# Kernel optimization log

Measured on AMD Instinct MI355X. Metric: run time of the kernel, lower is better.

Reference implementation:

```python
import jax, jax.numpy as jnp
import numpy as np

N = 100000
IN_DIM, H1, H2, OUT_DIM = 128, 128, 16, 10
DROP_P = 0.5


def setup_inputs() -> dict:
    key = jax.random.key(0)
    ks = jax.random.split(key, 9)
    x = jax.random.normal(ks[0], (N, IN_DIM), dtype=jnp.float32)
    edge_index = jax.random.randint(ks[1], (2, 1600000), 0, N, dtype=jnp.int64)
    s = lambda k, sh, fan: jax.random.normal(k, sh, jnp.float32) * (1.0 / np.sqrt(fan))
    return {
        "x": x,
        "edge_index": edge_index,
        "W1": s(ks[2], (IN_DIM, H1), IN_DIM),
        "b1": jnp.zeros((H1,), jnp.float32),
        "W2": s(ks[3], (H1, H2), H1),
        "b2": jnp.zeros((H2,), jnp.float32),
        "prelu_a": jnp.array(0.25, jnp.float32),  # nn.PReLU(): single shared parameter
        "Wfc": s(ks[4], (H2, OUT_DIM), H2),
        "bfc": jnp.zeros((OUT_DIM,), jnp.float32),
    }


def _prelu(x, a):
    return jnp.where(x >= 0, x, a * x)


def _dropout(x, key, p=DROP_P):
    keep = jax.random.bernoulli(key, 1.0 - p, x.shape)
    return jnp.where(keep, x / (1.0 - p), 0.0)


def _gcn_norm(edge_index, n):
    # PyG GCNConv default: add self-loops, symmetric deg^-1/2 normalization
    loop = jnp.arange(n, dtype=edge_index.dtype)
    src = jnp.concatenate([edge_index[0], loop])
    dst = jnp.concatenate([edge_index[1], loop])
    deg = jax.ops.segment_sum(jnp.ones_like(src, jnp.float32), dst, num_segments=n)
    dis = jnp.where(deg > 0, jax.lax.rsqrt(deg), 0.0)
    norm = dis[src] * dis[dst]  # [E + N]
    return src, dst, norm


def _gcn_conv(h, src, dst, norm, b, n):
    msg = h[src] * norm[:, None]          # gather + per-edge scale
    agg = jax.ops.segment_sum(msg, dst, num_segments=n)  # scatter-add
    return agg + b


def reference(x, edge_index, W1, b1, W2, b2, prelu_a, Wfc, bfc):
    n = x.shape[0]
    src, dst, norm = _gcn_norm(edge_index, n)
    dk1, dk2 = jax.random.split(jax.random.key(42))
    h = _gcn_conv(x @ W1, src, dst, norm, b1, n)
    h = _dropout(_prelu(h, prelu_a), dk1)
    h = _gcn_conv(h @ W2, src, dst, norm, b2, n)
    h = _dropout(_prelu(h, prelu_a), dk2)
    return h @ Wfc + bfc
```

## Files before the change

kernel.cpp:

```cpp
#include <hip/hip_runtime.h>
#include <stdint.h>

#define G1  128
#define BSH 9
#define BSZ 512

typedef __attribute__((ext_vector_type(8))) _Float16 f16x8;
typedef __attribute__((ext_vector_type(2))) _Float16 f16x2;
typedef __attribute__((ext_vector_type(2))) __fp16 fp16x2r;
typedef __attribute__((ext_vector_type(4))) float f32x4;

#define TF_ROUND(x0, x1, r)                                                    \
  {                                                                            \
    x0 += x1;                                                                  \
    x1 = (x1 << r) | (x1 >> (32 - r));                                         \
    x1 ^= x0;                                                                  \
  }

__host__ __device__ inline void threefry2x32(uint32_t k0, uint32_t k1,
                                             uint32_t x0, uint32_t x1,
                                             uint32_t* o0, uint32_t* o1) {
  uint32_t ks2 = k0 ^ k1 ^ 0x1BD11BDAu;
  x0 += k0; x1 += k1;
  TF_ROUND(x0, x1, 13) TF_ROUND(x0, x1, 15) TF_ROUND(x0, x1, 26) TF_ROUND(x0, x1, 6)
  x0 += k1; x1 += ks2 + 1u;
  TF_ROUND(x0, x1, 17) TF_ROUND(x0, x1, 29) TF_ROUND(x0, x1, 16) TF_ROUND(x0, x1, 24)
  x0 += ks2; x1 += k0 + 2u;
  TF_ROUND(x0, x1, 13) TF_ROUND(x0, x1, 15) TF_ROUND(x0, x1, 26) TF_ROUND(x0, x1, 6)
  x0 += k0; x1 += k1 + 3u;
  TF_ROUND(x0, x1, 17) TF_ROUND(x0, x1, 29) TF_ROUND(x0, x1, 16) TF_ROUND(x0, x1, 24)
  x0 += k1; x1 += ks2 + 4u;
  TF_ROUND(x0, x1, 13) TF_ROUND(x0, x1, 15) TF_ROUND(x0, x1, 26) TF_ROUND(x0, x1, 6)
  x0 += ks2; x1 += k0 + 5u;
  *o0 = x0; *o1 = x1;
}

__device__ inline uint32_t tf_bits32(uint32_t k0, uint32_t k1, uint32_t ctr) {
  uint32_t a, b;
  threefry2x32(k0, k1, 0u, ctr, &a, &b);
  return a ^ b;
}

__device__ inline f16x2 u2h(uint32_t u) {
  union { uint32_t u; f16x2 h; } c; c.u = u; return c.h;
}
__device__ inline uint32_t h2u(f16x2 h) {
  union { uint32_t u; f16x2 h; } c; c.h = h; return c.u;
}
__device__ inline uint32_t pk2h(float a, float b) {
  union { fp16x2r h; uint32_t u; } c;
  c.h = __builtin_amdgcn_cvt_pkrtz(a, b);
  return c.u;
}
__device__ inline uint16_t f2h(float a) {
  union { fp16x2r h; uint32_t u; } c;
  c.h = __builtin_amdgcn_cvt_pkrtz(a, 0.f);
  return (uint16_t)c.u;
}

__global__ __launch_bounds__(256) void k_hist(const int* __restrict__ dst,
                                              int* __restrict__ hist_t,
                                              int E, int NB, int chunk) {
  __shared__ int hist[256];
  const int tid = threadIdx.x;
  for (int b = tid; b < NB; b += 256) hist[b] = 0;
  __syncthreads();
  int e0 = blockIdx.x * chunk;
  int e1 = min(e0 + chunk, E);
  for (int e = e0 + tid; e < e1; e += 256)
    atomicAdd(&hist[dst[e] >> BSH], 1);
  __syncthreads();
  for (int b = tid; b < NB; b += 256)
    hist_t[b * G1 + blockIdx.x] = hist[b];
}

__global__ __launch_bounds__(256) void k_bsc_gemm1(
    const int* __restrict__ src, const int* __restrict__ dst,
    const int* __restrict__ hist_t, int* __restrict__ segs,
    uint32_t* __restrict__ ebuf, int E, int NB, int chunk,
    const float* __restrict__ x, const float* __restrict__ W,
    uint16_t* __restrict__ h, int n) {
  __shared__ char smem[(64 * 136 + 128 * 136) * 2];
  const int tid = threadIdx.x;
  if (blockIdx.x < G1) {
    int* rowsum = (int*)smem;
    int* cur = ((int*)smem) + 256;
    const int g = blockIdx.x;
    int rs = 0, ps = 0;
    if (tid < NB) {
      const int* row = hist_t + tid * G1;
      for (int i = 0; i < G1; ++i) {
        int v = row[i];
        rs += v;
        if (i < g) ps += v;
      }
    }
    rowsum[tid] = rs;
    __syncthreads();
    for (int off = 1; off < 256; off <<= 1) {
      int tmp = (tid >= off) ? rowsum[tid - off] : 0;
      __syncthreads();
      rowsum[tid] += tmp;
      __syncthreads();
    }
    int rb = rowsum[tid] - rs;
    if (tid < NB) cur[tid] = rb + ps;
    if (g == 0) {
      if (tid < NB) segs[tid] = rb;
      if (tid == 255) segs[NB] = rowsum[255];
    }
    __syncthreads();
    int e0 = g * chunk, e1 = min(e0 + chunk, E);
    for (int e = e0 + tid; e < e1; e += 256) {
      int d = dst[e];
      int slot = atomicAdd(&cur[d >> BSH], 1);
      ebuf[slot] = ((uint32_t)src[e] << BSH) | (uint32_t)(d & (BSZ - 1));
    }
    return;
  }
  uint16_t (*As)[136] = (uint16_t(*)[136])smem;
  uint16_t (*Bs)[136] = (uint16_t(*)[136])(smem + 64 * 136 * 2);
  const int rowBase = (blockIdx.x - G1) * 64;
  for (int i = tid; i < 64 * 32; i += 256) {
    int r = i >> 5, c4 = i & 31;
    float4 v = make_float4(0.f, 0.f, 0.f, 0.f);
    if (rowBase + r < n)
      v = ((const float4*)(x + (size_t)(rowBase + r) * 128))[c4];
    *(uint2*)&As[r][c4 * 4] = make_uint2(pk2h(v.x, v.y), pk2h(v.z, v.w));
  }
  {
    int k2 = tid >> 7;
    int c = tid & 127;
    for (int kk = 0; kk < 128; kk += 4) {
      int k = kk + k2 * 2;
      *(uint32_t*)&Bs[c][k] = pk2h(W[k * 128 + c], W[(k + 1) * 128 + c]);
    }
  }
  __syncthreads();
  const int wid = tid >> 6;
  const int lane = tid & 63;
  const int l15 = lane & 15;
  const int lhi = lane >> 4;
  f32x4 acc[8];
#pragma unroll
  for (int t = 0; t < 8; ++t) acc[t] = (f32x4){0.f, 0.f, 0.f, 0.f};
  const int arow = wid * 16 + l15;
#pragma unroll
  for (int ks = 0; ks < 4; ++ks) {
    f16x8 a = *(f16x8*)&As[arow][ks * 32 + lhi * 8];
#pragma unroll
    for (int ct = 0; ct < 8; ++ct) {
      f16x8 bfrag = *(f16x8*)&Bs[ct * 16 + l15][ks * 32 + lhi * 8];
      acc[ct] = __builtin_amdgcn_mfma_f32_16x16x32_f16(a, bfrag, acc[ct], 0, 0, 0);
    }
  }
#pragma unroll
  for (int j = 0; j < 4; ++j) {
    int row = rowBase + wid * 16 + lhi * 4 + j;
    if (row < n) {
#pragma unroll
      for (int ct = 0; ct < 8; ++ct)
        h[(size_t)row * 128 + ct * 16 + l15] = f2h(acc[ct][j]);
    }
  }
}

__global__ __launch_bounds__(256) void k_bfinal(const uint32_t* __restrict__ ebuf,
                                                const int* __restrict__ segs,
                                                int* __restrict__ rowptr,
                                                float* __restrict__ dis,
                                                int* __restrict__ csrc,
                                                int n, int NB, int E) {
  __shared__ int cnt[BSZ];
  __shared__ int sc[256];
  int b = blockIdx.x;
  int t = threadIdx.x;
  int seg0 = segs[b];
  int seg1 = segs[b + 1];
  for (int i = t; i < BSZ; i += 256) cnt[i] = 0;
  __syncthreads();
  for (int i = seg0 + t; i < seg1; i += 256)
    atomicAdd(&cnt[ebuf[i] & (BSZ - 1)], 1);
  __syncthreads();
  int a0 = cnt[2 * t], a1 = cnt[2 * t + 1];
  int s = a0 + a1;
  sc[t] = s;
  __syncthreads();
  for (int off = 1; off < 256; off <<= 1) {
    int tmp = (t >= off) ? sc[t - off] : 0;
    __syncthreads();
    sc[t] += tmp;
    __syncthreads();
  }
  int pre = sc[t] - s;
  int node0 = b * BSZ;
  int p0 = seg0 + pre;
  int p1 = p0 + a0;
  int nd0 = node0 + 2 * t, nd1 = nd0 + 1;
  if (nd0 <= n) rowptr[nd0] = p0;
  if (nd1 <= n) rowptr[nd1] = p1;
  if (nd0 < n) dis[nd0] = rsqrtf((float)(a0 + 1));
  if (nd1 < n) dis[nd1] = rsqrtf((float)(a1 + 1));
  cnt[2 * t] = p0;
  cnt[2 * t + 1] = p1;
  __syncthreads();
  for (int i = seg0 + t; i < seg1; i += 256) {
    uint32_t u = ebuf[i];
    int slot = atomicAdd(&cnt[u & (BSZ - 1)], 1);
    csrc[slot] = (int)(u >> BSH);
  }
  if (b == NB - 1 && t == 0) rowptr[n] = E;
}

__global__ __launch_bounds__(256) void k_gather12(
    const int* __restrict__ rowptr, const int* __restrict__ csrc,
    const float* __restrict__ dis, const uint16_t* __restrict__ h1,
    const float* __restrict__ bias, const float* __restrict__ pa,
    const float* __restrict__ W2, uint32_t* __restrict__ h2,
    int n, uint32_t k0, uint32_t k1) {
  __shared__ uint16_t hs[16][136];
  __shared__ uint16_t Bs[16][136];
  const int tid = threadIdx.x;
  {
    int c = tid & 15;
    int k8 = tid >> 4;
#pragma unroll
    for (int jj = 0; jj < 8; ++jj) {
      int k = k8 * 8 + jj;
      Bs[c][k] = f2h(W2[k * 16 + c]);
    }
  }
  const int wid = tid >> 6;
  const int lane = tid & 63;
  const int q = lane >> 4;
  const int sl = lane & 15;
  const int f0 = 8 * sl + 2 * q;
  const int base = blockIdx.x * 16;
  const uint4* rowbase = (const uint4*)h1;
  const float a = pa[0];
  const float bi0 = bias[f0];
  const float bi1 = bias[f0 + 1];
  for (int i = 0; i < 4; ++i) {
    const int nrow = wid * 4 + i;
    const int v = base + nrow;
    if (v < n) {
      uint32_t jj = (uint32_t)v * 128u + (uint32_t)f0;
      uint32_t bits0 = tf_bits32(k0, k1, jj);
      uint32_t bits1 = tf_bits32(k0, k1, jj + 1);
      float dv = dis[v];
      f16x2 acc0 = u2h(0u), acc1 = u2h(0u), acc2 = u2h(0u), acc3 = u2h(0u);
      if (q == 0) {
        uint4 r = rowbase[(size_t)v * 16 + sl];
        f16x2 w = u2h(pk2h(dv, dv));
        acc0 += u2h(r.x) * w; acc1 += u2h(r.y) * w;
        acc2 += u2h(r.z) * w; acc3 += u2h(r.w) * w;
      }
      int beg = rowptr[v];
      int deg = rowptr[v + 1] - beg;
      for (int bb = 0; bb < deg; bb += 64) {
        int cnt = min(64, deg - bb);
        int idx = bb + lane;
        int sv = v;
        uint32_t wpk = 0u;
        if (idx < deg) {
          sv = csrc[beg + idx];
          float wd = dis[sv];
          wpk = pk2h(wd, wd);
        }
        for (int j = 0; j < cnt; j += 16) {
          int s0 = __shfl(sv, j + q);
          int s1 = __shfl(sv, j + 4 + q);
          int s2 = __shfl(sv, j + 8 + q);
          int s3 = __shfl(sv, j + 12 + q);
          uint32_t w0 = (uint32_t)__shfl((int)wpk, j + q);
          uint32_t w1 = (uint32_t)__shfl((int)wpk, j + 4 + q);
          uint32_t w2 = (uint32_t)__shfl((int)wpk, j + 8 + q);
          uint32_t w3 = (uint32_t)__shfl((int)wpk, j + 12 + q);
          uint4 r0 = rowbase[(size_t)s0 * 16 + sl];
          uint4 r1 = rowbase[(size_t)s1 * 16 + sl];
          uint4 r2 = rowbase[(size_t)s2 * 16 + sl];
          uint4 r3 = rowbase[(size_t)s3 * 16 + sl];
          f16x2 hw0 = u2h(w0), hw1 = u2h(w1), hw2 = u2h(w2), hw3 = u2h(w3);
          acc0 += u2h(r0.x) * hw0; acc1 += u2h(r0.y) * hw0;
          acc2 += u2h(r0.z) * hw0; acc3 += u2h(r0.w) * hw0;
          acc0 += u2h(r1.x) * hw1; acc1 += u2h(r1.y) * hw1;
          acc2 += u2h(r1.z) * hw1; acc3 += u2h(r1.w) * hw1;
          acc0 += u2h(r2.x) * hw2; acc1 += u2h(r2.y) * hw2;
          acc2 += u2h(r2.z) * hw2; acc3 += u2h(r2.w) * hw2;
          acc0 += u2h(r3.x) * hw3; acc1 += u2h(r3.y) * hw3;
          acc2 += u2h(r3.z) * hw3; acc3 += u2h(r3.w) * hw3;
        }
      }
#define COMB(A)                                                                \
  {                                                                            \
    uint32_t u_ = h2u(A);                                                      \
    A = A + u2h((uint32_t)__shfl_xor((int)u_, 16));                            \
    u_ = h2u(A);                                                               \
    A = A + u2h((uint32_t)__shfl_xor((int)u_, 32));                            \
  }
      COMB(acc0) COMB(acc1) COMB(acc2) COMB(acc3)
#undef COMB
      f16x2 p = (q == 0) ? acc0 : (q == 1) ? acc1 : (q == 2) ? acc2 : acc3;
      float v0 = (float)p.x * dv + bi0;
      float v1 = (float)p.y * dv + bi1;
      v0 = v0 >= 0.f ? v0 : a * v0;
      v1 = v1 >= 0.f ? v1 : a * v1;
      float r0 = (bits0 & 0x80000000u) ? 0.f : 2.f * v0;
      float r1 = (bits1 & 0x80000000u) ? 0.f : 2.f * v1;
      *(uint32_t*)&hs[nrow][f0] = pk2h(r0, r1);
    } else {
      *(uint32_t*)&hs[nrow][f0] = 0u;
    }
  }
  __syncthreads();
  if (wid == 0) {
    const int l15 = lane & 15;
    const int lhi = lane >> 4;
    f32x4 acc = (f32x4){0.f, 0.f, 0.f, 0.f};
#pragma unroll
    for (int ks = 0; ks < 4; ++ks) {
      f16x8 af = *(f16x8*)&hs[l15][ks * 32 + lhi * 8];
      f16x8 bf = *(f16x8*)&Bs[l15][ks * 32 + lhi * 8];
      acc = __builtin_amdgcn_mfma_f32_16x16x32_f16(af, bf, acc, 0, 0, 0);
    }
#pragma unroll
    for (int j = 0; j < 4; ++j) {
      int gnode = base + lhi * 4 + j;
      float val = acc[j];
      float pv = __shfl_xor(val, 1);
      if (gnode < n && (l15 & 1) == 0)
        h2[(size_t)gnode * 8 + (l15 >> 1)] = pk2h(val, pv);
    }
  }
}

__global__ __launch_bounds__(256) void k_gather2(
    const int* __restrict__ rowptr, const int* __restrict__ csrc,
    const float* __restrict__ dis, const uint32_t* __restrict__ h2,
    const float* __restrict__ bias, const float* __restrict__ pa,
    const float* __restrict__ Wfc, const float* __restrict__ bfc,
    float* __restrict__ out, int n, uint32_t k0, uint32_t k1) {
  __shared__ float wfc[16][10];
  __shared__ float sbfc[10];
  __shared__ float sval[32][16];
  const int tid = threadIdx.x;
  if (tid < 160) ((float*)wfc)[tid] = Wfc[tid];
  if (tid < 10) sbfc[tid] = bfc[tid];
  __syncthreads();
  const int gnode = (blockIdx.x * 256 + tid) >> 3;
  const int grp = tid >> 3;
  const int sub = tid & 7;
  const int q = sub >> 1;
  const int sl = sub & 1;
  const int f0 = 8 * sl + 2 * q;
  const uint4* rowbase = (const uint4*)h2;
  if (gnode < n) {
    uint32_t c0 = (uint32_t)gnode * 16u + (uint32_t)f0;
    uint32_t bits0 = tf_bits32(k0, k1, c0);
    uint32_t bits1 = tf_bits32(k0, k1, c0 + 1);
    float dv = dis[gnode];
    f16x2 acc0 = u2h(0u), acc1 = u2h(0u), acc2 = u2h(0u), acc3 = u2h(0u);
    if (q == 0) {
      uint4 r = rowbase[(size_t)gnode * 2 + sl];
      f16x2 w = u2h(pk2h(dv, dv));
      acc0 += u2h(r.x) * w; acc1 += u2h(r.y) * w;
      acc2 += u2h(r.z) * w; acc3 += u2h(r.w) * w;
    }
    int beg = rowptr[gnode];
    int deg = rowptr[gnode + 1] - beg;
    for (int bb = 0; bb < deg; bb += 8) {
      int cnt = min(8, deg - bb);
      int idx = bb + sub;
      int sv = gnode;
      uint32_t wpk = 0u;
      if (idx < deg) {
        sv = csrc[beg + idx];
        float wd = dis[sv];
        wpk = pk2h(wd, wd);
      }
      for (int j = 0; j < cnt; j += 4) {
        int s0 = __shfl(sv, j + q, 8);
        uint32_t w0 = (uint32_t)__shfl((int)wpk, j + q, 8);
        uint4 r0 = rowbase[(size_t)s0 * 2 + sl];
        f16x2 hw0 = u2h(w0);
        acc0 += u2h(r0.x) * hw0; acc1 += u2h(r0.y) * hw0;
        acc2 += u2h(r0.z) * hw0; acc3 += u2h(r0.w) * hw0;
      }
    }
#define COMB2(A)                                                               \
  {                                                                            \
    uint32_t u_ = h2u(A);                                                      \
    A = A + u2h((uint32_t)__shfl_xor((int)u_, 2));                             \
    u_ = h2u(A);                                                               \
    A = A + u2h((uint32_t)__shfl_xor((int)u_, 4));                             \
  }
    COMB2(acc0) COMB2(acc1) COMB2(acc2) COMB2(acc3)
#undef COMB2
    f16x2 p = (q == 0) ? acc0 : (q == 1) ? acc1 : (q == 2) ? acc2 : acc3;
    float a = pa[0];
    float v0 = (float)p.x * dv + bias[f0];
    float v1 = (float)p.y * dv + bias[f0 + 1];
    v0 = v0 >= 0.f ? v0 : a * v0;
    v1 = v1 >= 0.f ? v1 : a * v1;
    sval[grp][f0]     = (bits0 & 0x80000000u) ? 0.f : 2.f * v0;
    sval[grp][f0 + 1] = (bits1 & 0x80000000u) ? 0.f : 2.f * v1;
  }
  __syncthreads();
  if (gnode < n && sub < 5) {
    int c = sub * 2;
    float o0 = sbfc[c], o1 = sbfc[c + 1];
#pragma unroll
    for (int k = 0; k < 16; ++k) {
      float hv = sval[grp][k];
      o0 += hv * wfc[k][c];
      o1 += hv * wfc[k][c + 1];
    }
    *(float2*)&out[(size_t)gnode * 10 + c] = make_float2(o0, o1);
  }
}

extern "C" void kernel_launch(void* const* d_in, const int* in_sizes, int n_in,
                              void* d_out, int out_size, void* d_ws, size_t ws_size,
                              hipStream_t stream) {
  const float* x   = (const float*)d_in[0];
  const int*   ei  = (const int*)d_in[1];
  const float* W1  = (const float*)d_in[2];
  const float* b1  = (const float*)d_in[3];
  const float* W2  = (const float*)d_in[4];
  const float* b2  = (const float*)d_in[5];
  const float* pa  = (const float*)d_in[6];
  const float* Wfc = (const float*)d_in[7];
  const float* bfc = (const float*)d_in[8];
  float* out = (float*)d_out;

  const int n = in_sizes[0] / 128;
  const int E = in_sizes[1] / 2;
  const int* src = ei;
  const int* dst = ei + E;

  const int NB = (n + BSZ - 1) / BSZ;
  const int T = NB * G1;
  const int chunk = (E + G1 - 1) / G1;

  char* w = (char*)d_ws;
  auto alloc = [&](size_t bytes) {
    char* p = w;
    w += (bytes + 255) & ~(size_t)255;
    return p;
  };
  float* dis      = (float*)alloc((size_t)n * 4);
  int* rowptr     = (int*)alloc((size_t)(n + 1) * 4);
  int* hist_t     = (int*)alloc((size_t)(T + 1) * 4);
  int* segs       = (int*)alloc((size_t)(NB + 1) * 4);
  uint32_t* ebuf  = (uint32_t*)alloc((size_t)E * 4);
  int* csrc       = (int*)alloc((size_t)E * 4);
  uint16_t* h1f   = (uint16_t*)alloc((size_t)n * 128 * 2);
  uint32_t* h2f   = (uint32_t*)alloc((size_t)n * 8 * 4);

  uint32_t dk1_0, dk1_1, dk2_0, dk2_1;
  threefry2x32(0u, 42u, 0u, 0u, &dk1_0, &dk1_1);
  threefry2x32(0u, 42u, 0u, 1u, &dk2_0, &dk2_1);

  k_hist<<<G1, 256, 0, stream>>>(dst, hist_t, E, NB, chunk);
  k_bsc_gemm1<<<G1 + (n + 63) / 64, 256, 0, stream>>>(
      src, dst, hist_t, segs, ebuf, E, NB, chunk, x, W1, h1f, n);
  k_bfinal<<<NB, 256, 0, stream>>>(ebuf, segs, rowptr, dis, csrc, n, NB, E);

  k_gather12<<<(n + 15) / 16, 256, 0, stream>>>(rowptr, csrc, dis, h1f,
                                                b1, pa, W2, h2f, n, dk1_0, dk1_1);

  k_gather2<<<(n * 8 + 255) / 256, 256, 0, stream>>>(rowptr, csrc, dis, h2f,
                                                     b2, pa, Wfc, bfc, out, n,
                                                     dk2_0, dk2_1);
}
```

Measured before the change: 169.6 us.

## Split layer-1 gather into feature-sliced kernel and separate MFMA GEMM2

Replaces the fused gather+GEMM2 kernel with two kernels. The first gathers neighbour rows in 8 feature slices of 16 features each, where 8-lane groups handle one node per slice, so each slice's working set of h1 is smaller and more likely to stay in cache. It applies bias, PReLU and dropout, then writes a full f16 hidden activation to a new global buffer. The second kernel loads 64-row tiles of that buffer and runs the 128x16 GEMM with MFMA on all four waves. This trades extra global traffic (an n x 128 f16 round trip) and an extra launch for better cache locality in the gather and no idle waves in the GEMM.

```diff
diff --git a/kernel.cpp b/kernel.cpp
--- a/kernel.cpp
+++ b/kernel.cpp
@@ -212,15 +212,92 @@
   if (b == NB - 1 && t == 0) rowptr[n] = E;
 }
 
-__global__ __launch_bounds__(256) void k_gather12(
+__global__ __launch_bounds__(256) void k_gslice(
     const int* __restrict__ rowptr, const int* __restrict__ csrc,
     const float* __restrict__ dis, const uint16_t* __restrict__ h1,
     const float* __restrict__ bias, const float* __restrict__ pa,
-    const float* __restrict__ W2, uint32_t* __restrict__ h2,
-    int n, uint32_t k0, uint32_t k1) {
-  __shared__ uint16_t hs[16][136];
+    uint32_t* __restrict__ hbf, int n, uint32_t k0, uint32_t k1) {
+  const int slice = blockIdx.x & 7;
+  const int nblk = blockIdx.x >> 3;
+  const int tid = threadIdx.x;
+  const int grp = tid >> 3;
+  const int sub = tid & 7;
+  const int q = sub >> 1;
+  const int sl = sub & 1;
+  const int fo = slice * 16 + sl * 8 + q * 2;
+  const float a = pa[0];
+  const float bi0 = bias[fo], bi1 = bias[fo + 1];
+  const uint4* rowbase = (const uint4*)h1;
+  const int roff = slice * 2 + sl;
+  for (int i = 0; i < 4; ++i) {
+    const int v = nblk * 128 + grp * 4 + i;
+    if (v >= n) break;
+    uint32_t cc = (uint32_t)v * 128u + (uint32_t)fo;
+    uint32_t bits0 = tf_bits32(k0, k1, cc);
+    uint32_t bits1 = tf_bits32(k0, k1, cc + 1);
+    float dv = dis[v];
+    f16x2 acc0 = u2h(0u), acc1 = u2h(0u), acc2 = u2h(0u), acc3 = u2h(0u);
+    if (q == 0) {
+      uint4 r = rowbase[(size_t)v * 16 + roff];
+      f16x2 w = u2h(pk2h(dv, dv));
+      acc0 += u2h(r.x) * w; acc1 += u2h(r.y) * w;
+      acc2 += u2h(r.z) * w; acc3 += u2h(r.w) * w;
+    }
+    int beg = rowptr[v];
+    int deg = rowptr[v + 1] - beg;
+    for (int bb = 0; bb < deg; bb += 8) {
+      int cnt = min(8, deg - bb);
+      int idx = bb + sub;
+      int sv = v;
+      uint32_t wpk = 0u;
+      if (idx < deg) {
+        sv = csrc[beg + idx];
+        float wd = dis[sv];
+        wpk = pk2h(wd, wd);
+      }
+      for (int j = 0; j < cnt; j += 4) {
+        int s0 = __shfl(sv, j + q, 8);
+        uint32_t w0 = (uint32_t)__shfl((int)wpk, j + q, 8);
+        uint4 r0 = rowbase[(size_t)s0 * 16 + roff];
+        f16x2 hw = u2h(w0);
+        acc0 += u2h(r0.x) * hw; acc1 += u2h(r0.y) * hw;
+        acc2 += u2h(r0.z) * hw; acc3 += u2h(r0.w) * hw;
+      }
+    }
+#define COMB2(A)                                                               \
+  {                                                                            \
+    uint32_t u_ = h2u(A);                                                      \
+    A = A + u2h((uint32_t)__shfl_xor((int)u_, 2));                             \
+    u_ = h2u(A);                                                               \
+    A = A + u2h((uint32_t)__shfl_xor((int)u_, 4));                             \
+  }
+    COMB2(acc0) COMB2(acc1) COMB2(acc2) COMB2(acc3)
+#undef COMB2
+    f16x2 p = (q == 0) ? acc0 : (q == 1) ? acc1 : (q == 2) ? acc2 : acc3;
+    float v0 = (float)p.x * dv + bi0;
+    float v1 = (float)p.y * dv + bi1;
+    v0 = v0 >= 0.f ? v0 : a * v0;
+    v1 = v1 >= 0.f ? v1 : a * v1;
+    float r0 = (bits0 & 0x80000000u) ? 0.f : 2.f * v0;
+    float r1 = (bits1 & 0x80000000u) ? 0.f : 2.f * v1;
+    hbf[(size_t)v * 64 + slice * 8 + sl * 4 + q] = pk2h(r0, r1);
+  }
+}
+
+__global__ __launch_bounds__(256) void k_gemm2(const uint32_t* __restrict__ hbf,
+                                               const float* __restrict__ W2,
+                                               uint32_t* __restrict__ h2, int n) {
+  __shared__ uint16_t As[64][136];
   __shared__ uint16_t Bs[16][136];
   const int tid = threadIdx.x;
+  const int rowBase = blockIdx.x * 64;
+  for (int i = tid; i < 64 * 32; i += 256) {
+    int r = i >> 5, c4 = i & 31;
+    uint2 v = make_uint2(0u, 0u);
+    if (rowBase + r < n)
+      v = ((const uint2*)(hbf + (size_t)(rowBase + r) * 64))[c4];
+    *(uint2*)&As[r][c4 * 4] = v;
+  }
   {
     int c = tid & 15;
     int k8 = tid >> 4;
@@ -230,107 +307,26 @@
       Bs[c][k] = f2h(W2[k * 16 + c]);
     }
   }
+  __syncthreads();
   const int wid = tid >> 6;
   const int lane = tid & 63;
-  const int q = lane >> 4;
-  const int sl = lane & 15;
-  const int f0 = 8 * sl + 2 * q;
-  const int base = blockIdx.x * 16;
-  const uint4* rowbase = (const uint4*)h1;
-  const float a = pa[0];
-  const float bi0 = bias[f0];
-  const float bi1 = bias[f0 + 1];
-  for (int i = 0; i < 4; ++i) {
-    const int nrow = wid * 4 + i;
-    const int v = base + nrow;
-    if (v < n) {
-      uint32_t jj = (uint32_t)v * 128u + (uint32_t)f0;
-      uint32_t bits0 = tf_bits32(k0, k1, jj);
-      uint32_t bits1 = tf_bits32(k0, k1, jj + 1);
-      float dv = dis[v];
-      f16x2 acc0 = u2h(0u), acc1 = u2h(0u), acc2 = u2h(0u), acc3 = u2h(0u);
-      if (q == 0) {
-        uint4 r = rowbase[(size_t)v * 16 + sl];
-        f16x2 w = u2h(pk2h(dv, dv));
-        acc0 += u2h(r.x) * w; acc1 += u2h(r.y) * w;
-        acc2 += u2h(r.z) * w; acc3 += u2h(r.w) * w;
-      }
-      int beg = rowptr[v];
-      int deg = rowptr[v + 1] - beg;
-      for (int bb = 0; bb < deg; bb += 64) {
-        int cnt = min(64, deg - bb);
-        int idx = bb + lane;
-        int sv = v;
-        uint32_t wpk = 0u;
-        if (idx < deg) {
-          sv = csrc[beg + idx];
-          float wd = dis[sv];
-          wpk = pk2h(wd, wd);
-        }
-        for (int j = 0; j < cnt; j += 16) {
-          int s0 = __shfl(sv, j + q);
-          int s1 = __shfl(sv, j + 4 + q);
-          int s2 = __shfl(sv, j + 8 + q);
-          int s3 = __shfl(sv, j + 12 + q);
-          uint32_t w0 = (uint32_t)__shfl((int)wpk, j + q);
-          uint32_t w1 = (uint32_t)__shfl((int)wpk, j + 4 + q);
-          uint32_t w2 = (uint32_t)__shfl((int)wpk, j + 8 + q);
-          uint32_t w3 = (uint32_t)__shfl((int)wpk, j + 12 + q);
-          uint4 r0 = rowbase[(size_t)s0 * 16 + sl];
-          uint4 r1 = rowbase[(size_t)s1 * 16 + sl];
-          uint4 r2 = rowbase[(size_t)s2 * 16 + sl];
-          uint4 r3 = rowbase[(size_t)s3 * 16 + sl];
-          f16x2 hw0 = u2h(w0), hw1 = u2h(w1), hw2 = u2h(w2), hw3 = u2h(w3);
-          acc0 += u2h(r0.x) * hw0; acc1 += u2h(r0.y) * hw0;
-          acc2 += u2h(r0.z) * hw0; acc3 += u2h(r0.w) * hw0;
-          acc0 += u2h(r1.x) * hw1; acc1 += u2h(r1.y) * hw1;
-          acc2 += u2h(r1.z) * hw1; acc3 += u2h(r1.w) * hw1;
-          acc0 += u2h(r2.x) * hw2; acc1 += u2h(r2.y) * hw2;
-          acc2 += u2h(r2.z) * hw2; acc3 += u2h(r2.w) * hw2;
-          acc0 += u2h(r3.x) * hw3; acc1 += u2h(r3.y) * hw3;
-          acc2 += u2h(r3.z) * hw3; acc3 += u2h(r3.w) * hw3;
-        }
-      }
-#define COMB(A)                                                                \
-  {                                                                            \
-    uint32_t u_ = h2u(A);                                                      \
-    A = A + u2h((uint32_t)__shfl_xor((int)u_, 16));                            \
-    u_ = h2u(A);                                                               \
-    A = A + u2h((uint32_t)__shfl_xor((int)u_, 32));                            \
-  }
-      COMB(acc0) COMB(acc1) COMB(acc2) COMB(acc3)
-#undef COMB
-      f16x2 p = (q == 0) ? acc0 : (q == 1) ? acc1 : (q == 2) ? acc2 : acc3;
-      float v0 = (float)p.x * dv + bi0;
-      float v1 = (float)p.y * dv + bi1;
-      v0 = v0 >= 0.f ? v0 : a * v0;
-      v1 = v1 >= 0.f ? v1 : a * v1;
-      float r0 = (bits0 & 0x80000000u) ? 0.f : 2.f * v0;
-      float r1 = (bits1 & 0x80000000u) ? 0.f : 2.f * v1;
-      *(uint32_t*)&hs[nrow][f0] = pk2h(r0, r1);
-    } else {
-      *(uint32_t*)&hs[nrow][f0] = 0u;
-    }
-  }
-  __syncthreads();
-  if (wid == 0) {
-    const int l15 = lane & 15;
-    const int lhi = lane >> 4;
-    f32x4 acc = (f32x4){0.f, 0.f, 0.f, 0.f};
-#pragma unroll
-    for (int ks = 0; ks < 4; ++ks) {
-      f16x8 af = *(f16x8*)&hs[l15][ks * 32 + lhi * 8];
-      f16x8 bf = *(f16x8*)&Bs[l15][ks * 32 + lhi * 8];
-      acc = __builtin_amdgcn_mfma_f32_16x16x32_f16(af, bf, acc, 0, 0, 0);
-    }
-#pragma unroll
-    for (int j = 0; j < 4; ++j) {
-      int gnode = base + lhi * 4 + j;
-      float val = acc[j];
-      float pv = __shfl_xor(val, 1);
-      if (gnode < n && (l15 & 1) == 0)
-        h2[(size_t)gnode * 8 + (l15 >> 1)] = pk2h(val, pv);
-    }
+  const int l15 = lane & 15;
+  const int lhi = lane >> 4;
+  f32x4 acc = (f32x4){0.f, 0.f, 0.f, 0.f};
+  const int arow = wid * 16 + l15;
+#pragma unroll
+  for (int ks = 0; ks < 4; ++ks) {
+    f16x8 a = *(f16x8*)&As[arow][ks * 32 + lhi * 8];
+    f16x8 bfrag = *(f16x8*)&Bs[l15][ks * 32 + lhi * 8];
+    acc = __builtin_amdgcn_mfma_f32_16x16x32_f16(a, bfrag, acc, 0, 0, 0);
+  }
+#pragma unroll
+  for (int j = 0; j < 4; ++j) {
+    int row = rowBase + wid * 16 + lhi * 4 + j;
+    float val = (row < n) ? acc[j] : 0.f;
+    float pv = __shfl_xor(val, 1);
+    if (row < n && (l15 & 1) == 0)
+      h2[(size_t)row * 8 + (l15 >> 1)] = pk2h(val, pv);
   }
 }
 
@@ -455,6 +451,7 @@
   uint32_t* ebuf  = (uint32_t*)alloc((size_t)E * 4);
   int* csrc       = (int*)alloc((size_t)E * 4);
   uint16_t* h1f   = (uint16_t*)alloc((size_t)n * 128 * 2);
+  uint32_t* hbf   = (uint32_t*)alloc((size_t)n * 64 * 4);
   uint32_t* h2f   = (uint32_t*)alloc((size_t)n * 8 * 4);
 
   uint32_t dk1_0, dk1_1, dk2_0, dk2_1;
@@ -466,8 +463,11 @@
       src, dst, hist_t, segs, ebuf, E, NB, chunk, x, W1, h1f, n);
   k_bfinal<<<NB, 256, 0, stream>>>(ebuf, segs, rowptr, dis, csrc, n, NB, E);
 
-  k_gather12<<<(n + 15) / 16, 256, 0, stream>>>(rowptr, csrc, dis, h1f,
-                                                b1, pa, W2, h2f, n, dk1_0, dk1_1);
+  const int nodeblocks = (n + 127) / 128;
+  k_gslice<<<8 * nodeblocks, 256, 0, stream>>>(rowptr, csrc, dis, h1f,
+                                               b1, pa, hbf, n, dk1_0, dk1_1);
+
+  k_gemm2<<<(n + 63) / 64, 256, 0, stream>>>(hbf, W2, h2f, n);
 
   k_gather2<<<(n * 8 + 255) / 256, 256, 0, stream>>>(rowptr, csrc, dis, h2f,
                                                      b2, pa, Wfc, bfc, out, n,
```

Result: slower. 359.6 us (+112.1%).
